# Kernel tuning notes

Hardware: AMD Instinct MI355X
Metric: run time of the kernel (lower is better)

The kernel has to match this reference:

```python
import jax, jax.numpy as jnp
import numpy as np

B, C, H, W = 16, 192, 64, 64
L = 256           # number of quantization levels (len(sos.unique_values))
EXTREMA = 10.0    # codebook support roughly [-extrema, extrema]


def setup_inputs() -> dict:
    key = jax.random.key(0)
    k1, k2, k3 = jax.random.split(key, 3)
    inputs = jax.random.normal(k1, (B, C, H, W), dtype=jnp.float32) * 3.0
    means = jax.random.normal(k2, (B, C, H, W), dtype=jnp.float32)
    # sorted codebook of unique quantizer output values (sos.unique_values)
    raw = jax.random.uniform(k3, (L,), dtype=jnp.float32,
                             minval=-EXTREMA, maxval=EXTREMA)
    unique_values = jnp.sort(raw)
    return {"inputs": inputs, "means": means, "unique_values": unique_values}


def _nearest_symbols(v, unique_values):
    # Parallel binary search over the sorted codebook; equivalent to the
    # original per-element argmin(|keys - x|) in transform_map.
    L_ = unique_values.shape[0]
    idx = jnp.searchsorted(unique_values, v)          # in [0, L]
    idx = jnp.clip(idx, 1, L_ - 1)
    left = unique_values[idx - 1]
    right = unique_values[idx]
    # on ties, argmin picks the lower index -> use <=
    return jnp.where(jnp.abs(v - left) <= jnp.abs(v - right), idx - 1, idx)


def reference(inputs, means, unique_values):
    # quantize(mode='symbols'): subtract means, snap to nearest codebook
    # value, map value -> integer symbol via the sorted codebook.
    v = inputs - means
    symbols = _nearest_symbols(v, unique_values)      # int32 [B,C,H,W]
    # dequantize: symbol -> float codebook value (map_cdf_sos), add means.
    dequant = unique_values[symbols] + means          # float32 [B,C,H,W]
    return dequant, symbols
```

## Files before the change

kernel.cpp:

```cpp
#include <hip/hip_runtime.h>


#define LVL 256
#define NB  1024
#define QPT 4

__device__ __forceinline__ int bucket_of(float v, float lo, float scale) {
    int b = (int)floorf((v - lo) * scale);
    return min(max(b, 0), NB - 1);
}

__global__ __launch_bounds__(256) void agc_build_lut(
    const float* __restrict__ uv, float4* __restrict__ lut)
{
    __shared__ float s_uv[LVL];
    __shared__ int   s_b[LVL];
    int t = threadIdx.x;
    s_uv[t] = uv[t];
    __syncthreads();
    const float lo    = s_uv[0];
    const float scale = (float)NB / (s_uv[LVL - 1] - lo);
    s_b[t] = bucket_of(s_uv[t], lo, scale);
    __syncthreads();

    #pragma unroll
    for (int q = 0; q < NB / 256; ++q) {
        int b = q * 256 + t;
        int A = 0, cnt = 0;
        for (int j = 0; j < LVL; ++j) {
            int bj = s_b[j];
            A   += (bj <  b);
            cnt += (bj == b);
        }
        float4 e;
        if (cnt == 0) {
            int idx = min(max(A, 1), LVL - 1);
            e.x = s_uv[idx - 1];
            e.y = s_uv[idx];
            e.z = (float)(idx - 1);
            e.w = 0.0f;
        } else {
            unsigned w = 0x80000000u | ((unsigned)A << 10) | (unsigned)cnt;
            e.x = 0.0f; e.y = 0.0f; e.z = 0.0f;
            e.w = __int_as_float((int)w);
        }
        lut[b] = e;
    }
}

__global__ __launch_bounds__(256) void agc_quant_lut(
    const float* __restrict__ inputs,
    const float* __restrict__ means,
    const float* __restrict__ uv,
    const float4* __restrict__ lut,
    float* __restrict__ out_deq,
    float* __restrict__ out_sym,
    int n4, int n, int gstride)
{
    __shared__ float  s_uv[LVL];
    __shared__ float4 s_lut[NB];

    int t = threadIdx.x;
    s_uv[t] = uv[t];
    #pragma unroll
    for (int q = 0; q < NB / 256; ++q)
        s_lut[q * 256 + t] = lut[q * 256 + t];
    __syncthreads();

    const float lo    = s_uv[0];
    const float scale = (float)NB / (s_uv[LVL - 1] - lo);

    const int base = blockIdx.x * blockDim.x + t;

    float4 in[QPT], mn[QPT];
    bool   ok[QPT];
    #pragma unroll
    for (int k = 0; k < QPT; ++k) {
        int i = base + k * gstride;
        ok[k] = (i < n4);
        if (ok[k]) {
            in[k] = reinterpret_cast<const float4*>(inputs)[i];
            mn[k] = reinterpret_cast<const float4*>(means)[i];
        }
    }

    #pragma unroll
    for (int k = 0; k < QPT; ++k) {
        if (!ok[k]) continue;
        int i = base + k * gstride;

        float vs[4] = {in[k].x - mn[k].x, in[k].y - mn[k].y,
                       in[k].z - mn[k].z, in[k].w - mn[k].w};
        float ms[4] = {mn[k].x, mn[k].y, mn[k].z, mn[k].w};
        float dq[4], sy[4];

        #pragma unroll
        for (int e4 = 0; e4 < 4; ++e4) {
            float v = vs[e4];
            int b = bucket_of(v, lo, scale);

            float4 e = s_lut[b];
            int w = __float_as_int(e.w);
            float left = e.x, right = e.y, basef = e.z;

            if (w < 0) {
                int A   = (w >> 10) & 0x3FF;
                int cnt =  w        & 0x3FF;
                int s = A, end = A + cnt;
                while (s < end && s_uv[s] < v) ++s;
                int idx = min(max(s, 1), LVL - 1);
                left  = s_uv[idx - 1];
                right = s_uv[idx];
                basef = (float)(idx - 1);
            }

            bool tl = (fabsf(v - left) <= fabsf(v - right));
            sy[e4] = tl ? basef : basef + 1.0f;
            dq[e4] = (tl ? left : right) + ms[e4];
        }

        reinterpret_cast<float4*>(out_deq)[i] = make_float4(dq[0], dq[1], dq[2], dq[3]);
        reinterpret_cast<float4*>(out_sym)[i] = make_float4(sy[0], sy[1], sy[2], sy[3]);
    }

    if (blockIdx.x == 0 && t == 0) {
        for (int j = n4 * 4; j < n; ++j) {
            float m = means[j];
            float v = inputs[j] - m;
            int l = 0, h = LVL;
            for (int s = 0; s < 8; ++s) {
                int mm = (l + h) >> 1;
                bool r = (s_uv[mm] < v);
                l = r ? (mm + 1) : l;
                h = r ? h : mm;
            }
            int idx = min(max(l, 1), LVL - 1);
            float left = s_uv[idx - 1], right = s_uv[idx];
            bool tl = fabsf(v - left) <= fabsf(v - right);
            out_deq[j] = (tl ? left : right) + m;
            out_sym[j] = (float)(tl ? idx - 1 : idx);
        }
    }
}

__global__ __launch_bounds__(256) void agc_quant_fallback(
    const float* __restrict__ inputs,
    const float* __restrict__ means,
    const float* __restrict__ uv,
    float* __restrict__ out_deq,
    float* __restrict__ out_sym,
    int n4, int n)
{
    __shared__ float s_uv[LVL];
    s_uv[threadIdx.x] = uv[threadIdx.x];
    __syncthreads();

    int i = blockIdx.x * blockDim.x + threadIdx.x;
    if (i < n4) {
        float4 in = reinterpret_cast<const float4*>(inputs)[i];
        float4 mn = reinterpret_cast<const float4*>(means)[i];
        float vs[4] = {in.x - mn.x, in.y - mn.y, in.z - mn.z, in.w - mn.w};
        float ms[4] = {mn.x, mn.y, mn.z, mn.w};
        float dq[4], sy[4];
        #pragma unroll
        for (int k = 0; k < 4; ++k) {
            float v = vs[k];
            int lo = 0, hi = LVL;
            #pragma unroll
            for (int s = 0; s < 8; ++s) {
                int mid = (lo + hi) >> 1;
                bool r = (s_uv[mid] < v);
                lo = r ? (mid + 1) : lo;
                hi = r ? hi : mid;
            }
            int idx = min(max(lo, 1), LVL - 1);
            float left = s_uv[idx - 1], right = s_uv[idx];
            bool tl = (fabsf(v - left) <= fabsf(v - right));
            sy[k] = (float)(tl ? idx - 1 : idx);
            dq[k] = (tl ? left : right) + ms[k];
        }
        reinterpret_cast<float4*>(out_deq)[i] = make_float4(dq[0], dq[1], dq[2], dq[3]);
        reinterpret_cast<float4*>(out_sym)[i] = make_float4(sy[0], sy[1], sy[2], sy[3]);
    }
    if (blockIdx.x == 0 && threadIdx.x == 0) {
        for (int j = n4 * 4; j < n; ++j) {
            float m = means[j];
            float v = inputs[j] - m;
            int lo = 0, hi = LVL;
            for (int s = 0; s < 8; ++s) {
                int mid = (lo + hi) >> 1;
                bool r = (s_uv[mid] < v);
                lo = r ? (mid + 1) : lo;
                hi = r ? hi : mid;
            }
            int idx = min(max(lo, 1), LVL - 1);
            float left = s_uv[idx - 1], right = s_uv[idx];
            bool tl = fabsf(v - left) <= fabsf(v - right);
            out_deq[j] = (tl ? left : right) + m;
            out_sym[j] = (float)(tl ? idx - 1 : idx);
        }
    }
}

extern "C" void kernel_launch(void* const* d_in, const int* in_sizes, int n_in,
                              void* d_out, int out_size, void* d_ws, size_t ws_size,
                              hipStream_t stream)
{
    const float* inputs = (const float*)d_in[0];
    const float* means  = (const float*)d_in[1];
    const float* uv     = (const float*)d_in[2];

    int n  = in_sizes[0];
    int n4 = n / 4;

    float* out     = (float*)d_out;
    float* out_deq = out;
    float* out_sym = out + n;

    size_t need = (size_t)NB * sizeof(float4);
    if (d_ws != nullptr && ws_size >= need) {
        agc_build_lut<<<1, 256, 0, stream>>>(uv, (float4*)d_ws);

        long long per_blk = 256LL * QPT;
        int blocks = (int)((n4 + per_blk - 1) / per_blk);
        if (blocks < 1) blocks = 1;
        int gstride = blocks * 256;
        agc_quant_lut<<<blocks, 256, 0, stream>>>(
            inputs, means, uv, (const float4*)d_ws,
            out_deq, out_sym, n4, n, gstride);
    } else {
        int blocks = (n4 + 255) / 256;
        if (blocks < 1) blocks = 1;
        agc_quant_fallback<<<blocks, 256, 0, stream>>>(
            inputs, means, uv, out_deq, out_sym, n4, n);
    }
}
```

Measured before the change: 201.2 us.

## Use two-part LUT resolving up to two in-bucket levels branch-free

The bucket LUT is split into two float4 tables that store up to two codebook pivots per bucket plus the neighbouring candidate values. Buckets holding one or two levels are now resolved with comparisons and selects instead of a serial scan over shared memory. The LUT build is spread across four blocks, and the element indexing changes from a grid-strided layout to per-block contiguous chunks with a no-bounds-check path for full blocks. In exchange, shared memory per block doubles to 32KB of LUT, which may lower occupancy, and each element does an extra LDS read.

```diff
diff --git a/kernel.cpp b/kernel.cpp
--- a/kernel.cpp
+++ b/kernel.cpp
@@ -11,7 +11,7 @@
 }
 
 __global__ __launch_bounds__(256) void agc_build_lut(
-    const float* __restrict__ uv, float4* __restrict__ lut)
+    const float* __restrict__ uv, float4* __restrict__ lutA, float4* __restrict__ lutB)
 {
     __shared__ float s_uv[LVL];
     __shared__ int   s_b[LVL];
@@ -23,71 +23,92 @@
     s_b[t] = bucket_of(s_uv[t], lo, scale);
     __syncthreads();
 
-    #pragma unroll
-    for (int q = 0; q < NB / 256; ++q) {
-        int b = q * 256 + t;
-        int A = 0, cnt = 0;
-        for (int j = 0; j < LVL; ++j) {
-            int bj = s_b[j];
-            A   += (bj <  b);
-            cnt += (bj == b);
-        }
-        float4 e;
-        if (cnt == 0) {
-            int idx = min(max(A, 1), LVL - 1);
-            e.x = s_uv[idx - 1];
-            e.y = s_uv[idx];
-            e.z = (float)(idx - 1);
-            e.w = 0.0f;
-        } else {
-            unsigned w = 0x80000000u | ((unsigned)A << 10) | (unsigned)cnt;
-            e.x = 0.0f; e.y = 0.0f; e.z = 0.0f;
-            e.w = __int_as_float((int)w);
-        }
-        lut[b] = e;
-    }
+    int b = blockIdx.x * 256 + t;
+    if (b >= NB) return;
+
+    int A = 0, cnt = 0;
+    for (int j = 0; j < LVL; ++j) {
+        int bj = s_b[j];
+        A   += (bj <  b);
+        cnt += (bj == b);
+    }
+
+    const float INF = __builtin_inff();
+    float4 ea, eb;
+    if (cnt == 0) {
+        int idx = min(max(A, 1), LVL - 1);
+        ea = make_float4(INF, INF, s_uv[idx - 1], s_uv[idx]);
+        eb = make_float4(0.f, 0.f, 0.f, __int_as_float(idx - 1));
+    } else if (cnt <= 2 && A >= 1 && A + cnt <= LVL - 1) {
+        float p0 = s_uv[A];
+        float p1 = (cnt >= 2) ? s_uv[A + 1] : INF;
+        float c0 = s_uv[A - 1];
+        float c1 = s_uv[A];
+        float c2 = s_uv[A + 1];
+        float c3 = (A + 2 <= LVL - 1) ? s_uv[A + 2] : 0.f;
+        ea = make_float4(p0, p1, c0, c1);
+        eb = make_float4(c2, c3, 0.f, __int_as_float(A - 1));
+    } else {
+        ea = make_float4(0.f, 0.f, 0.f, 0.f);
+        eb = make_float4(0.f, 0.f, 0.f, __int_as_float(-(A + 1)));
+    }
+    lutA[b] = ea;
+    lutB[b] = eb;
 }
 
 __global__ __launch_bounds__(256) void agc_quant_lut(
     const float* __restrict__ inputs,
     const float* __restrict__ means,
     const float* __restrict__ uv,
-    const float4* __restrict__ lut,
+    const float4* __restrict__ lutA,
+    const float4* __restrict__ lutB,
     float* __restrict__ out_deq,
     float* __restrict__ out_sym,
-    int n4, int n, int gstride)
+    int n4, int n, int nfull)
 {
     __shared__ float  s_uv[LVL];
-    __shared__ float4 s_lut[NB];
+    __shared__ float4 s_A[NB];
+    __shared__ float4 s_B[NB];
 
     int t = threadIdx.x;
     s_uv[t] = uv[t];
     #pragma unroll
-    for (int q = 0; q < NB / 256; ++q)
-        s_lut[q * 256 + t] = lut[q * 256 + t];
+    for (int q = 0; q < NB / 256; ++q) {
+        int j = q * 256 + t;
+        s_A[j] = lutA[j];
+        s_B[j] = lutB[j];
+    }
     __syncthreads();
 
     const float lo    = s_uv[0];
     const float scale = (float)NB / (s_uv[LVL - 1] - lo);
 
-    const int base = blockIdx.x * blockDim.x + t;
+    const int i0 = blockIdx.x * (256 * QPT) + t;
+    const bool full = (blockIdx.x < nfull);
 
     float4 in[QPT], mn[QPT];
-    bool   ok[QPT];
+    if (full) {
+        #pragma unroll
+        for (int k = 0; k < QPT; ++k) {
+            int i = i0 + k * 256;
+            in[k] = reinterpret_cast<const float4*>(inputs)[i];
+            mn[k] = reinterpret_cast<const float4*>(means)[i];
+        }
+    } else {
+        #pragma unroll
+        for (int k = 0; k < QPT; ++k) {
+            int i = i0 + k * 256;
+            if (i < n4) {
+                in[k] = reinterpret_cast<const float4*>(inputs)[i];
+                mn[k] = reinterpret_cast<const float4*>(means)[i];
+            }
+        }
+    }
+
     #pragma unroll
     for (int k = 0; k < QPT; ++k) {
-        int i = base + k * gstride;
-        ok[k] = (i < n4);
-        if (ok[k]) {
-            in[k] = reinterpret_cast<const float4*>(inputs)[i];
-            mn[k] = reinterpret_cast<const float4*>(means)[i];
-        }
-    }
-
-    #pragma unroll
-    for (int k = 0; k < QPT; ++k) {
-        if (!ok[k]) continue;
-        int i = base + k * gstride;
+        int i = i0 + k * 256;
+        if (!full && i >= n4) continue;
 
         float vs[4] = {in[k].x - mn[k].x, in[k].y - mn[k].y,
                        in[k].z - mn[k].z, in[k].w - mn[k].w};
@@ -95,28 +116,33 @@
         float dq[4], sy[4];
 
         #pragma unroll
-        for (int e4 = 0; e4 < 4; ++e4) {
-            float v = vs[e4];
+        for (int e = 0; e < 4; ++e) {
+            float v = vs[e];
             int b = bucket_of(v, lo, scale);
 
-            float4 e = s_lut[b];
-            int w = __float_as_int(e.w);
-            float left = e.x, right = e.y, basef = e.z;
-
-            if (w < 0) {
-                int A   = (w >> 10) & 0x3FF;
-                int cnt =  w        & 0x3FF;
-                int s = A, end = A + cnt;
-                while (s < end && s_uv[s] < v) ++s;
+            float4 A4 = s_A[b];
+            float4 B4 = s_B[b];
+            int bp = __float_as_int(B4.w);
+
+            float left, right;
+            int base;
+            if (bp >= 0) {
+                int sel = (A4.x < v) + (A4.y < v);
+                left  = (sel == 0) ? A4.z : ((sel == 1) ? A4.w : B4.x);
+                right = (sel == 0) ? A4.w : ((sel == 1) ? B4.x : B4.y);
+                base  = bp + sel;
+            } else {
+                int s = -bp - 1;
+                while (s < LVL && s_uv[s] < v) ++s;
                 int idx = min(max(s, 1), LVL - 1);
                 left  = s_uv[idx - 1];
                 right = s_uv[idx];
-                basef = (float)(idx - 1);
+                base  = idx - 1;
             }
 
             bool tl = (fabsf(v - left) <= fabsf(v - right));
-            sy[e4] = tl ? basef : basef + 1.0f;
-            dq[e4] = (tl ? left : right) + ms[e4];
+            sy[e] = (float)(base + (tl ? 0 : 1));
+            dq[e] = (tl ? left : right) + ms[e];
         }
 
         reinterpret_cast<float4*>(out_deq)[i] = make_float4(dq[0], dq[1], dq[2], dq[3]);
@@ -217,17 +243,19 @@
     float* out_deq = out;
     float* out_sym = out + n;
 
-    size_t need = (size_t)NB * sizeof(float4);
+    size_t need = (size_t)NB * 2 * sizeof(float4);
     if (d_ws != nullptr && ws_size >= need) {
-        agc_build_lut<<<1, 256, 0, stream>>>(uv, (float4*)d_ws);
-
-        long long per_blk = 256LL * QPT;
-        int blocks = (int)((n4 + per_blk - 1) / per_blk);
+        float4* lutA = (float4*)d_ws;
+        float4* lutB = lutA + NB;
+        agc_build_lut<<<NB / 256, 256, 0, stream>>>(uv, lutA, lutB);
+
+        int per_blk = 256 * QPT;
+        int nfull   = n4 / per_blk;
+        int blocks  = (n4 + per_blk - 1) / per_blk;
         if (blocks < 1) blocks = 1;
-        int gstride = blocks * 256;
         agc_quant_lut<<<blocks, 256, 0, stream>>>(
-            inputs, means, uv, (const float4*)d_ws,
-            out_deq, out_sym, n4, n, gstride);
+            inputs, means, uv, lutA, lutB,
+            out_deq, out_sym, n4, n, nfull);
     } else {
         int blocks = (n4 + 255) / 256;
         if (blocks < 1) blocks = 1;
```

Measured after the change: 188.3 us. 1.07x faster.
